# Performance work log

Hardware: AMD Instinct MI355X
Metric: run time of the kernel (lower is better)

The kernel has to match this reference:

```python
import jax, jax.numpy as jnp
import numpy as np

VOCAB = 256
BATCH = 524288
WORD_LEN = 16

# 7-d cross product structure constants (Fano plane triples, 1-indexed e_i)
_TRIPLES = [(1, 2, 3), (1, 4, 5), (1, 7, 6), (2, 4, 6), (2, 5, 7), (3, 4, 7), (3, 6, 5)]

def _build_C():
    C = np.zeros((7, 7, 7), dtype=np.float32)
    for (i, j, k) in _TRIPLES:
        i, j, k = i - 1, j - 1, k - 1
        # cyclic permutations +1, anti-cyclic -1
        for (a, b, c) in ((i, j, k), (j, k, i), (k, i, j)):
            C[a, b, c] = 1.0
        for (a, b, c) in ((j, i, k), (i, k, j), (k, j, i)):
            C[a, b, c] = -1.0
    return jnp.asarray(C)

_C = _build_C()

def _cross7(a, b):
    # a, b: (..., 7) -> (..., 7)
    return jnp.einsum('ijk,...i,...j->...k', _C, a, b)

def setup_inputs() -> dict:
    key = jax.random.key(0)
    k_ids, k_emb = jax.random.split(key)
    input_ids = jax.random.randint(k_ids, (BATCH, WORD_LEN), 0, VOCAB, dtype=jnp.int32)
    embedding = jax.random.normal(k_emb, (VOCAB, 8), dtype=jnp.float32)
    return {"input_ids": input_ids, "embedding": embedding}

def reference(input_ids, embedding):
    oct_emb = embedding[input_ids]          # (B, L, 8)
    imag = oct_emb[..., 1:]                 # (B, L, 7)
    init = imag[:, 0, :]                    # (B, 7)
    rest = jnp.swapaxes(imag[:, 1:, :], 0, 1)  # (L-1, B, 7)

    def step(v, x):
        return _cross7(v, x), None

    word_emb, _ = jax.lax.scan(step, init, rest)
    return word_emb                          # (B, 7)
```

## Files before the change

kernel.cpp:

```cpp
#include <hip/hip_runtime.h>

#define WORD_LEN 16
#define BLOCK 256
#define WPT 2

__device__ __forceinline__ void process_word(
    const float4* __restrict__ slo, const float4* __restrict__ shi,
    int4 w0, int4 w1, int4 w2, int4 w3, float* __restrict__ o)
{
    const int id[16] = {w0.x, w0.y, w0.z, w0.w,  w1.x, w1.y, w1.z, w1.w,
                        w2.x, w2.y, w2.z, w2.w,  w3.x, w3.y, w3.z, w3.w};

    float v0, v1, v2, v3, v4, v5, v6;
    {
        const float4 a = slo[id[0]];
        const float4 h = shi[id[0]];
        v0 = a.x; v1 = a.y; v2 = a.z; v3 = a.w;
        v4 = h.x; v5 = h.y; v6 = h.z;
    }

    #pragma unroll
    for (int t = 1; t < WORD_LEN; ++t) {
        const float4 a = shi ? slo[id[t]] : a;
        const float4 aa = slo[id[t]];
        const float4 hh = shi[id[t]];
        const float x0 = aa.x, x1 = aa.y, x2 = aa.z, x3 = aa.w;
        const float x4 = hh.x, x5 = hh.y, x6 = hh.z;

        float r0 = v1 * x2;  r0 = fmaf(-v2, x1, r0);  r0 = fmaf(v3, x4, r0);
        r0 = fmaf(-v4, x3, r0);  r0 = fmaf(v6, x5, r0);  r0 = fmaf(-v5, x6, r0);
        float r1 = v2 * x0;  r1 = fmaf(-v0, x2, r1);  r1 = fmaf(v3, x5, r1);
        r1 = fmaf(-v5, x3, r1);  r1 = fmaf(v4, x6, r1);  r1 = fmaf(-v6, x4, r1);
        float r2 = v0 * x1;  r2 = fmaf(-v1, x0, r2);  r2 = fmaf(v3, x6, r2);
        r2 = fmaf(-v6, x3, r2);  r2 = fmaf(v5, x4, r2);  r2 = fmaf(-v4, x5, r2);
        float r3 = v4 * x0;  r3 = fmaf(-v0, x4, r3);  r3 = fmaf(v5, x1, r3);
        r3 = fmaf(-v1, x5, r3);  r3 = fmaf(v6, x2, r3);  r3 = fmaf(-v2, x6, r3);
        float r4 = v0 * x3;  r4 = fmaf(-v3, x0, r4);  r4 = fmaf(v6, x1, r4);
        r4 = fmaf(-v1, x6, r4);  r4 = fmaf(v2, x5, r4);  r4 = fmaf(-v5, x2, r4);
        float r5 = v0 * x6;  r5 = fmaf(-v6, x0, r5);  r5 = fmaf(v1, x3, r5);
        r5 = fmaf(-v3, x1, r5);  r5 = fmaf(v4, x2, r5);  r5 = fmaf(-v2, x4, r5);
        float r6 = v5 * x0;  r6 = fmaf(-v0, x5, r6);  r6 = fmaf(v1, x4, r6);
        r6 = fmaf(-v4, x1, r6);  r6 = fmaf(v2, x3, r6);  r6 = fmaf(-v3, x2, r6);

        v0 = r0; v1 = r1; v2 = r2; v3 = r3; v4 = r4; v5 = r5; v6 = r6;
    }

    o[0] = v0; o[1] = v1; o[2] = v2; o[3] = v3; o[4] = v4; o[5] = v5; o[6] = v6;
}

__global__ __launch_bounds__(BLOCK, 4) void oct_word_emb_kernel(
    const int* __restrict__ ids,
    const float* __restrict__ emb,
    float* __restrict__ out)
{
    __shared__ float4 slo[256];
    __shared__ float4 shi[256];

    const int tid = threadIdx.x;
    {
        const float4* e4 = reinterpret_cast<const float4*>(emb);
        float4 lo = e4[tid * 2 + 0];
        float4 hi = e4[tid * 2 + 1];
        slo[tid] = make_float4(lo.y, lo.z, lo.w, hi.x);
        shi[tid] = make_float4(hi.y, hi.z, hi.w, 0.0f);
    }
    __syncthreads();

    const size_t wbase = (size_t)blockIdx.x * (BLOCK * WPT);
    const size_t wa = wbase + tid;
    const size_t wb = wbase + BLOCK + tid;

    const int4* ga = reinterpret_cast<const int4*>(ids) + wa * 4;
    const int4* gb = reinterpret_cast<const int4*>(ids) + wb * 4;
    const int4 a0 = ga[0], a1 = ga[1], a2 = ga[2], a3 = ga[3];
    const int4 b0 = gb[0], b1 = gb[1], b2 = gb[2], b3 = gb[3];

    process_word(slo, shi, a0, a1, a2, a3, out + wa * 7);
    process_word(slo, shi, b0, b1, b2, b3, out + wb * 7);
}

extern "C" void kernel_launch(void* const* d_in, const int* in_sizes, int n_in,
                              void* d_out, int out_size, void* d_ws, size_t ws_size,
                              hipStream_t stream) {
    const int* ids = (const int*)d_in[0];
    const float* emb = (const float*)d_in[1];
    float* out = (float*)d_out;

    const int batch = in_sizes[0] / WORD_LEN;
    const int grid = batch / (BLOCK * WPT);

    oct_word_emb_kernel<<<grid, BLOCK, 0, stream>>>(ids, emb, out);
}
```

Before: 17.98 us.

## Replicate embedding table eight times in LDS to cut bank conflicts on gathers

Builds eight copies of the 256-entry split embedding table in shared memory, interleaved so that each lane group reads its own copy. Random gathers from different lanes then spread across more banks and conflict less. The block grows to 512 threads with one word per thread instead of two per thread in 256-thread blocks. The cost is 64 KB of LDS per block, which may limit occupancy, plus a larger table fill before the barrier.

```diff
diff --git a/kernel.cpp b/kernel.cpp
--- a/kernel.cpp
+++ b/kernel.cpp
@@ -1,29 +1,56 @@
 #include <hip/hip_runtime.h>
 
 #define WORD_LEN 16
-#define BLOCK 256
-#define WPT 2
+#define BLOCK 512
 
-__device__ __forceinline__ void process_word(
-    const float4* __restrict__ slo, const float4* __restrict__ shi,
-    int4 w0, int4 w1, int4 w2, int4 w3, float* __restrict__ o)
+__global__ __launch_bounds__(BLOCK, 4) void oct_word_emb_kernel(
+    const int* __restrict__ ids,
+    const float* __restrict__ emb,
+    float* __restrict__ out)
 {
+    __shared__ float4 tab[256 * 16];
+
+    const int tid = threadIdx.x;
+
+    {
+        const int id = tid >> 1;
+        const int h  = tid & 1;
+        const float4* e4 = reinterpret_cast<const float4*>(emb);
+        float4 lo = e4[id * 2 + 0];
+        float4 hi = e4[id * 2 + 1];
+        const float4 val = h ? make_float4(hi.y, hi.z, hi.w, 0.0f)
+                             : make_float4(lo.y, lo.z, lo.w, hi.x);
+        const int base = id * 16 + h * 8;
+        #pragma unroll
+        for (int gg = 0; gg < 8; ++gg) {
+            const int g = (gg + tid) & 7;
+            tab[base + g] = val;
+        }
+    }
+    __syncthreads();
+
+    const int g = tid & 7;
+    const float4* mytab = tab + g;
+
+    const size_t w = (size_t)blockIdx.x * BLOCK + tid;
+
+    const int4* g4 = reinterpret_cast<const int4*>(ids) + w * 4;
+    const int4 w0 = g4[0], w1 = g4[1], w2 = g4[2], w3 = g4[3];
     const int id[16] = {w0.x, w0.y, w0.z, w0.w,  w1.x, w1.y, w1.z, w1.w,
                         w2.x, w2.y, w2.z, w2.w,  w3.x, w3.y, w3.z, w3.w};
 
     float v0, v1, v2, v3, v4, v5, v6;
     {
-        const float4 a = slo[id[0]];
-        const float4 h = shi[id[0]];
+        const float4 a = mytab[id[0] * 16];
+        const float4 h = mytab[id[0] * 16 + 8];
         v0 = a.x; v1 = a.y; v2 = a.z; v3 = a.w;
         v4 = h.x; v5 = h.y; v6 = h.z;
     }
 
     #pragma unroll
     for (int t = 1; t < WORD_LEN; ++t) {
-        const float4 a = shi ? slo[id[t]] : a;
-        const float4 aa = slo[id[t]];
-        const float4 hh = shi[id[t]];
+        const float4 aa = mytab[id[t] * 16];
+        const float4 hh = mytab[id[t] * 16 + 8];
         const float x0 = aa.x, x1 = aa.y, x2 = aa.z, x3 = aa.w;
         const float x4 = hh.x, x5 = hh.y, x6 = hh.z;
 
@@ -45,38 +72,8 @@
         v0 = r0; v1 = r1; v2 = r2; v3 = r3; v4 = r4; v5 = r5; v6 = r6;
     }
 
+    float* o = out + w * 7;
     o[0] = v0; o[1] = v1; o[2] = v2; o[3] = v3; o[4] = v4; o[5] = v5; o[6] = v6;
-}
-
-__global__ __launch_bounds__(BLOCK, 4) void oct_word_emb_kernel(
-    const int* __restrict__ ids,
-    const float* __restrict__ emb,
-    float* __restrict__ out)
-{
-    __shared__ float4 slo[256];
-    __shared__ float4 shi[256];
-
-    const int tid = threadIdx.x;
-    {
-        const float4* e4 = reinterpret_cast<const float4*>(emb);
-        float4 lo = e4[tid * 2 + 0];
-        float4 hi = e4[tid * 2 + 1];
-        slo[tid] = make_float4(lo.y, lo.z, lo.w, hi.x);
-        shi[tid] = make_float4(hi.y, hi.z, hi.w, 0.0f);
-    }
-    __syncthreads();
-
-    const size_t wbase = (size_t)blockIdx.x * (BLOCK * WPT);
-    const size_t wa = wbase + tid;
-    const size_t wb = wbase + BLOCK + tid;
-
-    const int4* ga = reinterpret_cast<const int4*>(ids) + wa * 4;
-    const int4* gb = reinterpret_cast<const int4*>(ids) + wb * 4;
-    const int4 a0 = ga[0], a1 = ga[1], a2 = ga[2], a3 = ga[3];
-    const int4 b0 = gb[0], b1 = gb[1], b2 = gb[2], b3 = gb[3];
-
-    process_word(slo, shi, a0, a1, a2, a3, out + wa * 7);
-    process_word(slo, shi, b0, b1, b2, b3, out + wb * 7);
 }
 
 extern "C" void kernel_launch(void* const* d_in, const int* in_sizes, int n_in,
@@ -87,7 +84,7 @@
     float* out = (float*)d_out;
 
     const int batch = in_sizes[0] / WORD_LEN;
-    const int grid = batch / (BLOCK * WPT);
+    const int grid = batch / BLOCK;
 
     oct_word_emb_kernel<<<grid, BLOCK, 0, stream>>>(ids, emb, out);
 }
```

Result: slower. 18.73 us (+4.2%).
